# Kernel optimization log

Hardware: AMD Instinct MI355X
Metric: run time of the kernel (lower is better)

## Reference

```python
import jax, jax.numpy as jnp
import numpy as np

B, T, H, I, O = 256, 8192, 16, 1, 1


def setup_inputs() -> dict:
    key = jax.random.key(0)
    ks = jax.random.split(key, 8)
    s = 1.0 / np.sqrt(H)  # PyTorch default init scale
    x = jax.random.normal(ks[0], (B, T, I), dtype=jnp.float32)
    h0 = jax.random.normal(ks[1], (1, B, H), dtype=jnp.float32)
    W_ih = jax.random.uniform(ks[2], (H, I), jnp.float32, -s, s)
    W_hh = jax.random.uniform(ks[3], (H, H), jnp.float32, -s, s)
    b_ih = jax.random.uniform(ks[4], (H,), jnp.float32, -s, s)
    b_hh = jax.random.uniform(ks[5], (H,), jnp.float32, -s, s)
    W_out = jax.random.uniform(ks[6], (O, H), jnp.float32, -s, s)
    b_out = jax.random.uniform(ks[7], (O,), jnp.float32, -s, s)
    return {"x": x, "h0": h0, "W_ih": W_ih, "W_hh": W_hh,
            "b_ih": b_ih, "b_hh": b_hh, "W_out": W_out, "b_out": b_out}


def reference(x, h0, W_ih, W_hh, b_ih, b_hh, W_out, b_out):
    # Precompute input projection for all timesteps: [T, B, H]
    xp = jnp.einsum('bti,hi->tbh', x, W_ih) + b_ih + b_hh

    def step(h, xt):
        h_new = jnp.tanh(xt + h @ W_hh.T)  # [B, H]
        return h_new, h_new

    hT, outs = jax.lax.scan(step, h0[0], xp)  # hT: [B,H], outs: [T,B,H]
    out_flat = outs.transpose(1, 0, 2).reshape(-1, H)  # [B*T, H]
    out = (out_flat @ W_out.T + b_out)[None]  # [1, B*T, O]
    return out, hT[None]  # hidden: [1, B, H]
```

## Files before the change

### kernel.cpp

```cpp
#include <hip/hip_runtime.h>

#define ROTI(v, CTRL) __builtin_amdgcn_update_dpp(0, (v), (CTRL), 0xF, 0xF, true)
#define ROTF(x, CTRL) __int_as_float(__builtin_amdgcn_update_dpp(0, __float_as_int(x), (CTRL), 0xF, 0xF, true))

constexpr int T_LEN = 8192;
constexpr int BATCH = 256;
constexpr int HID   = 16;

#define MATVEC(a0_, a1_, a2_, a3_, p_, h_)                                              \
  asm("s_nop 1\n\t"                                                                     \
      "v_fmac_f32 %[a0], %[h], %[w0]\n\t"                                               \
      "v_mul_f32_dpp %[a1], %[h], %[w4] row_ror:4 row_mask:0xf bank_mask:0xf\n\t"       \
      "v_mul_f32_dpp %[a2], %[h], %[w8] row_ror:8 row_mask:0xf bank_mask:0xf\n\t"       \
      "v_mul_f32_dpp %[a3], %[h], %[w12] row_ror:12 row_mask:0xf bank_mask:0xf\n\t"     \
      "v_add_f32_dpp %[p], %[p], %[p] row_ror:8 row_mask:0xf bank_mask:0xf\n\t"         \
      "v_fmac_f32_dpp %[a0], %[h], %[w1] row_ror:1 row_mask:0xf bank_mask:0xf\n\t"      \
      "v_fmac_f32_dpp %[a1], %[h], %[w5] row_ror:5 row_mask:0xf bank_mask:0xf\n\t"      \
      "v_fmac_f32_dpp %[a2], %[h], %[w9] row_ror:9 row_mask:0xf bank_mask:0xf\n\t"      \
      "v_add_f32_dpp %[p], %[p], %[p] row_ror:4 row_mask:0xf bank_mask:0xf\n\t"         \
      "v_fmac_f32_dpp %[a3], %[h], %[w13] row_ror:13 row_mask:0xf bank_mask:0xf\n\t"    \
      "v_fmac_f32_dpp %[a0], %[h], %[w2] row_ror:2 row_mask:0xf bank_mask:0xf\n\t"      \
      "v_fmac_f32_dpp %[a1], %[h], %[w6] row_ror:6 row_mask:0xf bank_mask:0xf\n\t"      \
      "v_add_f32_dpp %[p], %[p], %[p] row_ror:2 row_mask:0xf bank_mask:0xf\n\t"         \
      "v_fmac_f32_dpp %[a2], %[h], %[w10] row_ror:10 row_mask:0xf bank_mask:0xf\n\t"    \
      "v_fmac_f32_dpp %[a3], %[h], %[w14] row_ror:14 row_mask:0xf bank_mask:0xf\n\t"    \
      "v_fmac_f32_dpp %[a0], %[h], %[w3] row_ror:3 row_mask:0xf bank_mask:0xf\n\t"      \
      "v_add_f32_dpp %[p], %[p], %[p] row_ror:1 row_mask:0xf bank_mask:0xf\n\t"         \
      "v_fmac_f32_dpp %[a1], %[h], %[w7] row_ror:7 row_mask:0xf bank_mask:0xf\n\t"      \
      "v_fmac_f32_dpp %[a2], %[h], %[w11] row_ror:11 row_mask:0xf bank_mask:0xf\n\t"    \
      "v_fmac_f32_dpp %[a3], %[h], %[w15] row_ror:15 row_mask:0xf bank_mask:0xf\n\t"    \
      : [a0]"+v"(a0_), [a1]"=&v"(a1_), [a2]"=&v"(a2_), [a3]"=&v"(a3_), [p]"+v"(p_)     \
      : [h]"v"(h_),                                                                     \
        [w0]"v"(wr[0]),  [w1]"v"(wr[1]),  [w2]"v"(wr[2]),  [w3]"v"(wr[3]),              \
        [w4]"v"(wr[4]),  [w5]"v"(wr[5]),  [w6]"v"(wr[6]),  [w7]"v"(wr[7]),              \
        [w8]"v"(wr[8]),  [w9]"v"(wr[9]),  [w10]"v"(wr[10]), [w11]"v"(wr[11]),           \
        [w12]"v"(wr[12]), [w13]"v"(wr[13]), [w14]"v"(wr[14]), [w15]"v"(wr[15]))

#define STEP(XV, LSEL) do {                                                             \
    float a0 = fmaf((XV), wih, bias), a1, a2, a3;                                       \
    MATVEC(a0, a1, a2, a3, p, h);                                                       \
    float o = p + bo;                                                                   \
    osel = (j == (LSEL)) ? o : osel;                                                    \
    float s = (a0 + a1) + (a2 + a3);                                                    \
    float e = __expf(s + s);                                                            \
    h = fmaf(-2.0f, __builtin_amdgcn_rcpf(e + 1.0f), 1.0f);                             \
    p = h * wout;                                                                       \
} while (0)

__global__ void __launch_bounds__(64, 1)
rnn_fused(const float* __restrict__ x,
          const float* __restrict__ h0,
          const float* __restrict__ Wih,
          const float* __restrict__ Whh,
          const float* __restrict__ bih,
          const float* __restrict__ bhh,
          const float* __restrict__ Wout,
          const float* __restrict__ boutp,
          float* __restrict__ out)
{
    const int lane = (int)threadIdx.x;
    const int j    = lane & 15;
    const int b    = (int)blockIdx.x * 4 + (lane >> 4);

    const int pr  = ROTI(j, 0x121);
    const int dir = (__builtin_amdgcn_readfirstlane(pr) == 1) ? 1 : -1;

    float wr[16];
#pragma unroll
    for (int r = 0; r < 16; ++r)
        wr[r] = Whh[j * HID + ((j + dir * r) & 15)];

    const float wih  = Wih[j];
    const float bias = bih[j] + bhh[j];
    const float wout = Wout[j];
    const float bo   = boutp[0];

    float h = h0[b * HID + j];
    float p = h * wout;
    float osel = 0.0f;

    const float* xb = x   + (size_t)b * T_LEN;
    float*       ob = out + (size_t)b * T_LEN;

    const float4* xv4 = (const float4*)xb;
    float4 c0 = xv4[0], c1 = xv4[1], c2 = xv4[2], c3 = xv4[3];

    for (int t = 0; t < T_LEN; t += 16) {
        const float4* nx = (const float4*)(xb + ((t + 16) & (T_LEN - 1)));
        float4 n0 = nx[0], n1 = nx[1], n2 = nx[2], n3 = nx[3];

        STEP(c0.x, 15);
        if (t > 0)
            ob[t - 16 + j] = osel;
        STEP(c0.y, 0);
        STEP(c0.z, 1);
        STEP(c0.w, 2);
        STEP(c1.x, 3);
        STEP(c1.y, 4);
        STEP(c1.z, 5);
        STEP(c1.w, 6);
        STEP(c2.x, 7);
        STEP(c2.y, 8);
        STEP(c2.z, 9);
        STEP(c2.w, 10);
        STEP(c3.x, 11);
        STEP(c3.y, 12);
        STEP(c3.z, 13);
        STEP(c3.w, 14);

        c0 = n0; c1 = n1; c2 = n2; c3 = n3;
    }

    p += ROTF(p, 0x128);
    p += ROTF(p, 0x124);
    p += ROTF(p, 0x122);
    p += ROTF(p, 0x121);
    float o_last = p + bo;
    osel = (j == 15) ? o_last : osel;
    ob[T_LEN - 16 + j] = osel;

    out[(size_t)BATCH * T_LEN + (size_t)b * HID + j] = h;
}

extern "C" void kernel_launch(void* const* d_in, const int* in_sizes, int n_in,
                              void* d_out, int out_size, void* d_ws, size_t ws_size,
                              hipStream_t stream)
{
    const float* x    = (const float*)d_in[0];
    const float* h0   = (const float*)d_in[1];
    const float* Wih  = (const float*)d_in[2];
    const float* Whh  = (const float*)d_in[3];
    const float* bih  = (const float*)d_in[4];
    const float* bhh  = (const float*)d_in[5];
    const float* Wout = (const float*)d_in[6];
    const float* bout = (const float*)d_in[7];
    float* out = (float*)d_out;

    rnn_fused<<<dim3(BATCH / 4), dim3(64), 0, stream>>>(
        x, h0, Wih, Whh, bih, bhh, Wout, bout, out);
}
```

Before: 599.0 us.

## Interleave four batch groups per wavefront to hide recurrence latency

Each 64-lane wavefront now processes four independent groups of four batch rows, interleaving their matvec/tanh chains within every timestep, and the grid is reduced accordingly. Input prefetch uses ping-pong register buffers and tanh uses exp2 with a prescaled argument. The goal is to fill the DPP/transcendental latency bubbles of a single serial recurrence with independent work, at the cost of using far fewer CUs and more registers per wave.

```diff
diff --git a/kernel.cpp b/kernel.cpp
--- a/kernel.cpp
+++ b/kernel.cpp
@@ -6,6 +6,7 @@
 constexpr int T_LEN = 8192;
 constexpr int BATCH = 256;
 constexpr int HID   = 16;
+constexpr int G     = 4;
 
 #define MATVEC(a0_, a1_, a2_, a3_, p_, h_)                                              \
   asm("s_nop 1\n\t"                                                                     \
@@ -36,17 +37,6 @@
         [w8]"v"(wr[8]),  [w9]"v"(wr[9]),  [w10]"v"(wr[10]), [w11]"v"(wr[11]),           \
         [w12]"v"(wr[12]), [w13]"v"(wr[13]), [w14]"v"(wr[14]), [w15]"v"(wr[15]))
 
-#define STEP(XV, LSEL) do {                                                             \
-    float a0 = fmaf((XV), wih, bias), a1, a2, a3;                                       \
-    MATVEC(a0, a1, a2, a3, p, h);                                                       \
-    float o = p + bo;                                                                   \
-    osel = (j == (LSEL)) ? o : osel;                                                    \
-    float s = (a0 + a1) + (a2 + a3);                                                    \
-    float e = __expf(s + s);                                                            \
-    h = fmaf(-2.0f, __builtin_amdgcn_rcpf(e + 1.0f), 1.0f);                             \
-    p = h * wout;                                                                       \
-} while (0)
-
 __global__ void __launch_bounds__(64, 1)
 rnn_fused(const float* __restrict__ x,
           const float* __restrict__ h0,
@@ -60,7 +50,7 @@
 {
     const int lane = (int)threadIdx.x;
     const int j    = lane & 15;
-    const int b    = (int)blockIdx.x * 4 + (lane >> 4);
+    const int g    = lane >> 4;
 
     const int pr  = ROTI(j, 0x121);
     const int dir = (__builtin_amdgcn_readfirstlane(pr) == 1) ? 1 : -1;
@@ -75,51 +65,84 @@
     const float wout = Wout[j];
     const float bo   = boutp[0];
 
-    float h = h0[b * HID + j];
-    float p = h * wout;
-    float osel = 0.0f;
-
-    const float* xb = x   + (size_t)b * T_LEN;
-    float*       ob = out + (size_t)b * T_LEN;
-
-    const float4* xv4 = (const float4*)xb;
-    float4 c0 = xv4[0], c1 = xv4[1], c2 = xv4[2], c3 = xv4[3];
-
-    for (int t = 0; t < T_LEN; t += 16) {
-        const float4* nx = (const float4*)(xb + ((t + 16) & (T_LEN - 1)));
-        float4 n0 = nx[0], n1 = nx[1], n2 = nx[2], n3 = nx[3];
-
-        STEP(c0.x, 15);
-        if (t > 0)
-            ob[t - 16 + j] = osel;
-        STEP(c0.y, 0);
-        STEP(c0.z, 1);
-        STEP(c0.w, 2);
-        STEP(c1.x, 3);
-        STEP(c1.y, 4);
-        STEP(c1.z, 5);
-        STEP(c1.w, 6);
-        STEP(c2.x, 7);
-        STEP(c2.y, 8);
-        STEP(c2.z, 9);
-        STEP(c2.w, 10);
-        STEP(c3.x, 11);
-        STEP(c3.y, 12);
-        STEP(c3.z, 13);
-        STEP(c3.w, 14);
-
-        c0 = n0; c1 = n1; c2 = n2; c3 = n3;
+    int    b[G];
+    float  h[G], p[G], osel[G];
+    const float* xb[G];
+    float*       ob[G];
+#pragma unroll
+    for (int s = 0; s < G; ++s) {
+        b[s]    = (int)blockIdx.x * 16 + s * 4 + g;
+        h[s]    = h0[b[s] * HID + j];
+        p[s]    = h[s] * wout;
+        osel[s] = 0.0f;
+        xb[s]   = x   + (size_t)b[s] * T_LEN;
+        ob[s]   = out + (size_t)b[s] * T_LEN;
     }
 
-    p += ROTF(p, 0x128);
-    p += ROTF(p, 0x124);
-    p += ROTF(p, 0x122);
-    p += ROTF(p, 0x121);
-    float o_last = p + bo;
-    osel = (j == 15) ? o_last : osel;
-    ob[T_LEN - 16 + j] = osel;
+    float bufA[G][16], bufB[G][16];
+#pragma unroll
+    for (int s = 0; s < G; ++s)
+#pragma unroll
+        for (int q = 0; q < 4; ++q) {
+            float4 v = *(const float4*)(xb[s] + 4 * q);
+            bufA[s][4*q+0] = v.x; bufA[s][4*q+1] = v.y;
+            bufA[s][4*q+2] = v.z; bufA[s][4*q+3] = v.w;
+        }
 
-    out[(size_t)BATCH * T_LEN + (size_t)b * HID + j] = h;
+    auto body = [&](int t, float (&cur)[G][16], float (&nxt)[G][16]) {
+        const int tn = (t + 16) & (T_LEN - 1);
+#pragma unroll
+        for (int s = 0; s < G; ++s)
+#pragma unroll
+            for (int q = 0; q < 4; ++q) {
+                float4 v = *(const float4*)(xb[s] + tn + 4 * q);
+                nxt[s][4*q+0] = v.x; nxt[s][4*q+1] = v.y;
+                nxt[s][4*q+2] = v.z; nxt[s][4*q+3] = v.w;
+            }
+
+#pragma unroll
+        for (int pos = 0; pos < 16; ++pos) {
+            const int LSEL = (pos + 15) & 15;
+            float a0[G], a1[G], a2[G], a3[G];
+#pragma unroll
+            for (int s = 0; s < G; ++s) {
+                a0[s] = fmaf(cur[s][pos], wih, bias);
+                MATVEC(a0[s], a1[s], a2[s], a3[s], p[s], h[s]);
+            }
+#pragma unroll
+            for (int s = 0; s < G; ++s) {
+                float o = p[s] + bo;
+                osel[s] = (j == LSEL) ? o : osel[s];
+                float sum = (a0[s] + a1[s]) + (a2[s] + a3[s]);
+                float e   = __builtin_amdgcn_exp2f(sum * 2.8853900817779268f);
+                h[s] = fmaf(-2.0f, __builtin_amdgcn_rcpf(e + 1.0f), 1.0f);
+                p[s] = h[s] * wout;
+            }
+            if (pos == 0 && t > 0) {
+#pragma unroll
+                for (int s = 0; s < G; ++s)
+                    ob[s][t - 16 + j] = osel[s];
+            }
+        }
+    };
+
+    for (int t = 0; t < T_LEN; t += 32) {
+        body(t,      bufA, bufB);
+        body(t + 16, bufB, bufA);
+    }
+
+#pragma unroll
+    for (int s = 0; s < G; ++s) {
+        float q = p[s];
+        q += ROTF(q, 0x128);
+        q += ROTF(q, 0x124);
+        q += ROTF(q, 0x122);
+        q += ROTF(q, 0x121);
+        float o_last = q + bo;
+        osel[s] = (j == 15) ? o_last : osel[s];
+        ob[s][T_LEN - 16 + j] = osel[s];
+        out[(size_t)BATCH * T_LEN + (size_t)b[s] * HID + j] = h[s];
+    }
 }
 
 extern "C" void kernel_launch(void* const* d_in, const int* in_sizes, int n_in,
@@ -136,6 +159,6 @@
     const float* bout = (const float*)d_in[7];
     float* out = (float*)d_out;
 
-    rnn_fused<<<dim3(BATCH / 4), dim3(64), 0, stream>>>(
+    rnn_fused<<<dim3(BATCH / 16), dim3(64), 0, stream>>>(
         x, h0, Wih, Whh, bih, bhh, Wout, bout, out);
 }
```

Result: slower. 2.140 ms (+257.2%).

## Interleave two independent batch chains per wavefront to hide recurrence latency

Applied to the files above, without the earlier changes.

Each wavefront now carries two independent recurrent chains (batches b and b+4) and interleaves their matvec, tanh and output steps, so one chain's dependent DPP and transcendental latency can overlap with the other's work. The grid is halved to 32 blocks, so fewer CUs are in use but each has more instruction-level parallelism. The time loop is unrolled by 32 with double-buffered input prefetch, and exp is computed directly with exp2 using a prescaled constant. The risk is that with only one wave per CU, the halved parallelism makes the serial chain per wave twice as long if the interleaving does not hide enough latency.

```diff
diff --git a/kernel.cpp b/kernel.cpp
--- a/kernel.cpp
+++ b/kernel.cpp
@@ -31,25 +31,53 @@
       "v_fmac_f32_dpp %[a3], %[h], %[w15] row_ror:15 row_mask:0xf bank_mask:0xf\n\t"    \
       : [a0]"+v"(a0_), [a1]"=&v"(a1_), [a2]"=&v"(a2_), [a3]"=&v"(a3_), [p]"+v"(p_)     \
       : [h]"v"(h_),                                                                     \
-        [w0]"v"(wr[0]),  [w1]"v"(wr[1]),  [w2]"v"(wr[2]),  [w3]"v"(wr[3]),              \
-        [w4]"v"(wr[4]),  [w5]"v"(wr[5]),  [w6]"v"(wr[6]),  [w7]"v"(wr[7]),              \
-        [w8]"v"(wr[8]),  [w9]"v"(wr[9]),  [w10]"v"(wr[10]), [w11]"v"(wr[11]),           \
-        [w12]"v"(wr[12]), [w13]"v"(wr[13]), [w14]"v"(wr[14]), [w15]"v"(wr[15]))
+        [w0]"v"(wr0),  [w1]"v"(wr1),  [w2]"v"(wr2),  [w3]"v"(wr3),                      \
+        [w4]"v"(wr4),  [w5]"v"(wr5),  [w6]"v"(wr6),  [w7]"v"(wr7),                      \
+        [w8]"v"(wr8),  [w9]"v"(wr9),  [w10]"v"(wr10), [w11]"v"(wr11),                   \
+        [w12]"v"(wr12), [w13]"v"(wr13), [w14]"v"(wr14), [w15]"v"(wr15))
 
-#define STEP(XV, LSEL) do {                                                             \
-    float a0 = fmaf((XV), wih, bias), a1, a2, a3;                                       \
-    MATVEC(a0, a1, a2, a3, p, h);                                                       \
-    float o = p + bo;                                                                   \
-    osel = (j == (LSEL)) ? o : osel;                                                    \
-    float s = (a0 + a1) + (a2 + a3);                                                    \
-    float e = __expf(s + s);                                                            \
-    h = fmaf(-2.0f, __builtin_amdgcn_rcpf(e + 1.0f), 1.0f);                             \
-    p = h * wout;                                                                       \
+#define STEP2(XV0, XV1, LSEL) do {                                                      \
+    float a00 = fmaf((XV0), wih, bias), a10, a20, a30;                                  \
+    float a01 = fmaf((XV1), wih, bias), a11, a21, a31;                                  \
+    MATVEC(a00, a10, a20, a30, p0, hh0);                                                \
+    MATVEC(a01, a11, a21, a31, p1, hh1);                                                \
+    float o0 = p0 + bo;                                                                 \
+    float o1 = p1 + bo;                                                                 \
+    osel0 = (j == (LSEL)) ? o0 : osel0;                                                 \
+    osel1 = (j == (LSEL)) ? o1 : osel1;                                                 \
+    float s0 = (a00 + a10) + (a20 + a30);                                               \
+    float s1 = (a01 + a11) + (a21 + a31);                                               \
+    float e0 = __builtin_amdgcn_exp2f(s0 * 2.8853900817779268f);                        \
+    float e1 = __builtin_amdgcn_exp2f(s1 * 2.8853900817779268f);                        \
+    hh0 = fmaf(-2.0f, __builtin_amdgcn_rcpf(e0 + 1.0f), 1.0f);                          \
+    hh1 = fmaf(-2.0f, __builtin_amdgcn_rcpf(e1 + 1.0f), 1.0f);                          \
+    p0 = hh0 * wout;                                                                    \
+    p1 = hh1 * wout;                                                                    \
+} while (0)
+
+#define BLOCK16(tb, Q0, Q1, Q2, Q3, R0, R1, R2, R3) do {                                \
+    STEP2(Q0.x, R0.x, 15);                                                              \
+    if ((tb) > 0) { ob0[(tb) - 16 + j] = osel0; ob1[(tb) - 16 + j] = osel1; }           \
+    STEP2(Q0.y, R0.y, 0);                                                               \
+    STEP2(Q0.z, R0.z, 1);                                                               \
+    STEP2(Q0.w, R0.w, 2);                                                               \
+    STEP2(Q1.x, R1.x, 3);                                                               \
+    STEP2(Q1.y, R1.y, 4);                                                               \
+    STEP2(Q1.z, R1.z, 5);                                                               \
+    STEP2(Q1.w, R1.w, 6);                                                               \
+    STEP2(Q2.x, R2.x, 7);                                                               \
+    STEP2(Q2.y, R2.y, 8);                                                               \
+    STEP2(Q2.z, R2.z, 9);                                                               \
+    STEP2(Q2.w, R2.w, 10);                                                              \
+    STEP2(Q3.x, R3.x, 11);                                                              \
+    STEP2(Q3.y, R3.y, 12);                                                              \
+    STEP2(Q3.z, R3.z, 13);                                                              \
+    STEP2(Q3.w, R3.w, 14);                                                              \
 } while (0)
 
 __global__ void __launch_bounds__(64, 1)
 rnn_fused(const float* __restrict__ x,
-          const float* __restrict__ h0,
+          const float* __restrict__ hinit,
           const float* __restrict__ Wih,
           const float* __restrict__ Whh,
           const float* __restrict__ bih,
@@ -60,66 +88,92 @@
 {
     const int lane = (int)threadIdx.x;
     const int j    = lane & 15;
-    const int b    = (int)blockIdx.x * 4 + (lane >> 4);
+    const int g    = lane >> 4;
 
     const int pr  = ROTI(j, 0x121);
     const int dir = (__builtin_amdgcn_readfirstlane(pr) == 1) ? 1 : -1;
 
-    float wr[16];
-#pragma unroll
-    for (int r = 0; r < 16; ++r)
-        wr[r] = Whh[j * HID + ((j + dir * r) & 15)];
+    float wr0  = Whh[j * HID + ((j + dir * 0)  & 15)];
+    float wr1  = Whh[j * HID + ((j + dir * 1)  & 15)];
+    float wr2  = Whh[j * HID + ((j + dir * 2)  & 15)];
+    float wr3  = Whh[j * HID + ((j + dir * 3)  & 15)];
+    float wr4  = Whh[j * HID + ((j + dir * 4)  & 15)];
+    float wr5  = Whh[j * HID + ((j + dir * 5)  & 15)];
+    float wr6  = Whh[j * HID + ((j + dir * 6)  & 15)];
+    float wr7  = Whh[j * HID + ((j + dir * 7)  & 15)];
+    float wr8  = Whh[j * HID + ((j + dir * 8)  & 15)];
+    float wr9  = Whh[j * HID + ((j + dir * 9)  & 15)];
+    float wr10 = Whh[j * HID + ((j + dir * 10) & 15)];
+    float wr11 = Whh[j * HID + ((j + dir * 11) & 15)];
+    float wr12 = Whh[j * HID + ((j + dir * 12) & 15)];
+    float wr13 = Whh[j * HID + ((j + dir * 13) & 15)];
+    float wr14 = Whh[j * HID + ((j + dir * 14) & 15)];
+    float wr15 = Whh[j * HID + ((j + dir * 15) & 15)];
 
     const float wih  = Wih[j];
     const float bias = bih[j] + bhh[j];
     const float wout = Wout[j];
     const float bo   = boutp[0];
 
-    float h = h0[b * HID + j];
-    float p = h * wout;
-    float osel = 0.0f;
+    const int b0 = (int)blockIdx.x * 8 + g;
+    const int b1 = b0 + 4;
 
-    const float* xb = x   + (size_t)b * T_LEN;
-    float*       ob = out + (size_t)b * T_LEN;
+    float hh0 = hinit[b0 * HID + j];
+    float hh1 = hinit[b1 * HID + j];
+    float p0 = hh0 * wout;
+    float p1 = hh1 * wout;
+    float osel0 = 0.0f, osel1 = 0.0f;
 
-    const float4* xv4 = (const float4*)xb;
-    float4 c0 = xv4[0], c1 = xv4[1], c2 = xv4[2], c3 = xv4[3];
+    const float* xb0 = x   + (size_t)b0 * T_LEN;
+    const float* xb1 = x   + (size_t)b1 * T_LEN;
+    float*       ob0 = out + (size_t)b0 * T_LEN;
+    float*       ob1 = out + (size_t)b1 * T_LEN;
 
-    for (int t = 0; t < T_LEN; t += 16) {
-        const float4* nx = (const float4*)(xb + ((t + 16) & (T_LEN - 1)));
-        float4 n0 = nx[0], n1 = nx[1], n2 = nx[2], n3 = nx[3];
+    float4 A0 = ((const float4*)xb0)[0], A1 = ((const float4*)xb0)[1],
+           A2 = ((const float4*)xb0)[2], A3 = ((const float4*)xb0)[3];
+    float4 C0 = ((const float4*)xb1)[0], C1 = ((const float4*)xb1)[1],
+           C2 = ((const float4*)xb1)[2], C3 = ((const float4*)xb1)[3];
+    float4 B0, B1, B2, B3, D0, D1, D2, D3;
 
-        STEP(c0.x, 15);
-        if (t > 0)
-            ob[t - 16 + j] = osel;
-        STEP(c0.y, 0);
-        STEP(c0.z, 1);
-        STEP(c0.w, 2);
-        STEP(c1.x, 3);
-        STEP(c1.y, 4);
-        STEP(c1.z, 5);
-        STEP(c1.w, 6);
-        STEP(c2.x, 7);
-        STEP(c2.y, 8);
-        STEP(c2.z, 9);
-        STEP(c2.w, 10);
-        STEP(c3.x, 11);
-        STEP(c3.y, 12);
-        STEP(c3.z, 13);
-        STEP(c3.w, 14);
+    for (int t = 0; t < T_LEN; t += 32) {
+        {
+            const float* q0 = xb0 + t + 16;
+            const float* q1 = xb1 + t + 16;
+            B0 = ((const float4*)q0)[0]; B1 = ((const float4*)q0)[1];
+            B2 = ((const float4*)q0)[2]; B3 = ((const float4*)q0)[3];
+            D0 = ((const float4*)q1)[0]; D1 = ((const float4*)q1)[1];
+            D2 = ((const float4*)q1)[2]; D3 = ((const float4*)q1)[3];
+        }
+        BLOCK16(t, A0, A1, A2, A3, C0, C1, C2, C3);
 
-        c0 = n0; c1 = n1; c2 = n2; c3 = n3;
+        {
+            const int tn = (t + 32) & (T_LEN - 1);
+            const float* q0 = xb0 + tn;
+            const float* q1 = xb1 + tn;
+            A0 = ((const float4*)q0)[0]; A1 = ((const float4*)q0)[1];
+            A2 = ((const float4*)q0)[2]; A3 = ((const float4*)q0)[3];
+            C0 = ((const float4*)q1)[0]; C1 = ((const float4*)q1)[1];
+            C2 = ((const float4*)q1)[2]; C3 = ((const float4*)q1)[3];
+        }
+        BLOCK16(t + 16, B0, B1, B2, B3, D0, D1, D2, D3);
     }
 
-    p += ROTF(p, 0x128);
-    p += ROTF(p, 0x124);
-    p += ROTF(p, 0x122);
-    p += ROTF(p, 0x121);
-    float o_last = p + bo;
-    osel = (j == 15) ? o_last : osel;
-    ob[T_LEN - 16 + j] = osel;
-
-    out[(size_t)BATCH * T_LEN + (size_t)b * HID + j] = h;
+    {
+        float q = p0;
+        q += ROTF(q, 0x128); q += ROTF(q, 0x124);
+        q += ROTF(q, 0x122); q += ROTF(q, 0x121);
+        osel0 = (j == 15) ? (q + bo) : osel0;
+        ob0[T_LEN - 16 + j] = osel0;
+        out[(size_t)BATCH * T_LEN + (size_t)b0 * HID + j] = hh0;
+    }
+    {
+        float q = p1;
+        q += ROTF(q, 0x128); q += ROTF(q, 0x124);
+        q += ROTF(q, 0x122); q += ROTF(q, 0x121);
+        osel1 = (j == 15) ? (q + bo) : osel1;
+        ob1[T_LEN - 16 + j] = osel1;
+        out[(size_t)BATCH * T_LEN + (size_t)b1 * HID + j] = hh1;
+    }
 }
 
 extern "C" void kernel_launch(void* const* d_in, const int* in_sizes, int n_in,
@@ -136,6 +190,6 @@
     const float* bout = (const float*)d_in[7];
     float* out = (float*)d_out;
 
-    rnn_fused<<<dim3(BATCH / 4), dim3(64), 0, stream>>>(
+    rnn_fused<<<dim3(BATCH / 8), dim3(64), 0, stream>>>(
         x, h0, Wih, Whh, bih, bhh, Wout, bout, out);
 }
```

New measurement: 1.093 ms. 1.82x slower.

## Offload output projection to a consumer wavefront via an LDS ring buffer

Applied to the files above, without the earlier changes.

Splits each block into a producer wavefront that runs the recurrence and a consumer wavefront that computes the output projection. Hidden states pass between them through a shared-memory ring buffer with spin-wait counters. This takes the per-step DPP reduction and output select off the serial critical path. It also folds the 2*log2(e) factor into the weights so tanh can use exp2 directly. The cost is LDS stores on every step, spin-wait synchronisation, and a second wavefront competing for issue slots.

```diff
diff --git a/kernel.cpp b/kernel.cpp
--- a/kernel.cpp
+++ b/kernel.cpp
@@ -1,55 +1,58 @@
 #include <hip/hip_runtime.h>
 
 #define ROTI(v, CTRL) __builtin_amdgcn_update_dpp(0, (v), (CTRL), 0xF, 0xF, true)
-#define ROTF(x, CTRL) __int_as_float(__builtin_amdgcn_update_dpp(0, __float_as_int(x), (CTRL), 0xF, 0xF, true))
 
-constexpr int T_LEN = 8192;
-constexpr int BATCH = 256;
-constexpr int HID   = 16;
+constexpr int T_LEN  = 8192;
+constexpr int BATCH  = 256;
+constexpr int HID    = 16;
+constexpr int RING   = 128;
+constexpr int SLOT_W = 68;
+constexpr int CHUNK  = 32;
 
-#define MATVEC(a0_, a1_, a2_, a3_, p_, h_)                                              \
+#define MATVEC(a0_, a1_, a2_, a3_, h_)                                                  \
   asm("s_nop 1\n\t"                                                                     \
       "v_fmac_f32 %[a0], %[h], %[w0]\n\t"                                               \
       "v_mul_f32_dpp %[a1], %[h], %[w4] row_ror:4 row_mask:0xf bank_mask:0xf\n\t"       \
       "v_mul_f32_dpp %[a2], %[h], %[w8] row_ror:8 row_mask:0xf bank_mask:0xf\n\t"       \
       "v_mul_f32_dpp %[a3], %[h], %[w12] row_ror:12 row_mask:0xf bank_mask:0xf\n\t"     \
-      "v_add_f32_dpp %[p], %[p], %[p] row_ror:8 row_mask:0xf bank_mask:0xf\n\t"         \
       "v_fmac_f32_dpp %[a0], %[h], %[w1] row_ror:1 row_mask:0xf bank_mask:0xf\n\t"      \
       "v_fmac_f32_dpp %[a1], %[h], %[w5] row_ror:5 row_mask:0xf bank_mask:0xf\n\t"      \
       "v_fmac_f32_dpp %[a2], %[h], %[w9] row_ror:9 row_mask:0xf bank_mask:0xf\n\t"      \
-      "v_add_f32_dpp %[p], %[p], %[p] row_ror:4 row_mask:0xf bank_mask:0xf\n\t"         \
       "v_fmac_f32_dpp %[a3], %[h], %[w13] row_ror:13 row_mask:0xf bank_mask:0xf\n\t"    \
       "v_fmac_f32_dpp %[a0], %[h], %[w2] row_ror:2 row_mask:0xf bank_mask:0xf\n\t"      \
       "v_fmac_f32_dpp %[a1], %[h], %[w6] row_ror:6 row_mask:0xf bank_mask:0xf\n\t"      \
-      "v_add_f32_dpp %[p], %[p], %[p] row_ror:2 row_mask:0xf bank_mask:0xf\n\t"         \
       "v_fmac_f32_dpp %[a2], %[h], %[w10] row_ror:10 row_mask:0xf bank_mask:0xf\n\t"    \
       "v_fmac_f32_dpp %[a3], %[h], %[w14] row_ror:14 row_mask:0xf bank_mask:0xf\n\t"    \
       "v_fmac_f32_dpp %[a0], %[h], %[w3] row_ror:3 row_mask:0xf bank_mask:0xf\n\t"      \
-      "v_add_f32_dpp %[p], %[p], %[p] row_ror:1 row_mask:0xf bank_mask:0xf\n\t"         \
       "v_fmac_f32_dpp %[a1], %[h], %[w7] row_ror:7 row_mask:0xf bank_mask:0xf\n\t"      \
       "v_fmac_f32_dpp %[a2], %[h], %[w11] row_ror:11 row_mask:0xf bank_mask:0xf\n\t"    \
       "v_fmac_f32_dpp %[a3], %[h], %[w15] row_ror:15 row_mask:0xf bank_mask:0xf\n\t"    \
-      : [a0]"+v"(a0_), [a1]"=&v"(a1_), [a2]"=&v"(a2_), [a3]"=&v"(a3_), [p]"+v"(p_)     \
+      : [a0]"+v"(a0_), [a1]"=&v"(a1_), [a2]"=&v"(a2_), [a3]"=&v"(a3_)                  \
       : [h]"v"(h_),                                                                     \
-        [w0]"v"(wr[0]),  [w1]"v"(wr[1]),  [w2]"v"(wr[2]),  [w3]"v"(wr[3]),              \
-        [w4]"v"(wr[4]),  [w5]"v"(wr[5]),  [w6]"v"(wr[6]),  [w7]"v"(wr[7]),              \
-        [w8]"v"(wr[8]),  [w9]"v"(wr[9]),  [w10]"v"(wr[10]), [w11]"v"(wr[11]),           \
-        [w12]"v"(wr[12]), [w13]"v"(wr[13]), [w14]"v"(wr[14]), [w15]"v"(wr[15]))
+        [w0]"v"(wr0),  [w1]"v"(wr1),  [w2]"v"(wr2),  [w3]"v"(wr3),                      \
+        [w4]"v"(wr4),  [w5]"v"(wr5),  [w6]"v"(wr6),  [w7]"v"(wr7),                      \
+        [w8]"v"(wr8),  [w9]"v"(wr9),  [w10]"v"(wr10), [w11]"v"(wr11),                   \
+        [w12]"v"(wr12), [w13]"v"(wr13), [w14]"v"(wr14), [w15]"v"(wr15))
 
-#define STEP(XV, LSEL) do {                                                             \
-    float a0 = fmaf((XV), wih, bias), a1, a2, a3;                                       \
-    MATVEC(a0, a1, a2, a3, p, h);                                                       \
-    float o = p + bo;                                                                   \
-    osel = (j == (LSEL)) ? o : osel;                                                    \
+#define STEP(XV) do {                                                                   \
+    float a0 = fmaf((XV), wihK, biasK), a1, a2, a3;                                     \
+    MATVEC(a0, a1, a2, a3, h);                                                          \
     float s = (a0 + a1) + (a2 + a3);                                                    \
-    float e = __expf(s + s);                                                            \
+    float e = __builtin_amdgcn_exp2f(s);                                                \
     h = fmaf(-2.0f, __builtin_amdgcn_rcpf(e + 1.0f), 1.0f);                             \
-    p = h * wout;                                                                       \
+    *rp = h; rp += SLOT_W;                                                              \
 } while (0)
 
-__global__ void __launch_bounds__(64, 1)
+#define BLOCK16(C0, C1, C2, C3) do {                                                    \
+    STEP(C0.x); STEP(C0.y); STEP(C0.z); STEP(C0.w);                                     \
+    STEP(C1.x); STEP(C1.y); STEP(C1.z); STEP(C1.w);                                     \
+    STEP(C2.x); STEP(C2.y); STEP(C2.z); STEP(C2.w);                                     \
+    STEP(C3.x); STEP(C3.y); STEP(C3.z); STEP(C3.w);                                     \
+} while (0)
+
+__global__ void __launch_bounds__(128, 1)
 rnn_fused(const float* __restrict__ x,
-          const float* __restrict__ h0,
+          const float* __restrict__ hinit,
           const float* __restrict__ Wih,
           const float* __restrict__ Whh,
           const float* __restrict__ bih,
@@ -58,68 +61,115 @@
           const float* __restrict__ boutp,
           float* __restrict__ out)
 {
-    const int lane = (int)threadIdx.x;
-    const int j    = lane & 15;
-    const int b    = (int)blockIdx.x * 4 + (lane >> 4);
+    __shared__ float ring[RING * SLOT_W];
+    __shared__ int   syncc[2];
+    volatile int* prodc = &syncc[0];
+    volatile int* consc = &syncc[1];
 
-    const int pr  = ROTI(j, 0x121);
-    const int dir = (__builtin_amdgcn_readfirstlane(pr) == 1) ? 1 : -1;
+    const int tid = (int)threadIdx.x;
+    if (tid == 0) { syncc[0] = 0; syncc[1] = 0; }
+    __syncthreads();
 
-    float wr[16];
-#pragma unroll
-    for (int r = 0; r < 16; ++r)
-        wr[r] = Whh[j * HID + ((j + dir * r) & 15)];
+    if (tid < 64) {
+        const int j = tid & 15;
+        const int g = tid >> 4;
+        const int b = (int)blockIdx.x * 4 + g;
 
-    const float wih  = Wih[j];
-    const float bias = bih[j] + bhh[j];
-    const float wout = Wout[j];
-    const float bo   = boutp[0];
+        const int pr  = ROTI(j, 0x121);
+        const int dir = (__builtin_amdgcn_readfirstlane(pr) == 1) ? 1 : -1;
 
-    float h = h0[b * HID + j];
-    float p = h * wout;
-    float osel = 0.0f;
+        const float K2 = 2.8853900817779268f;
+        float wr0  = K2 * Whh[j * HID + ((j + dir * 0)  & 15)];
+        float wr1  = K2 * Whh[j * HID + ((j + dir * 1)  & 15)];
+        float wr2  = K2 * Whh[j * HID + ((j + dir * 2)  & 15)];
+        float wr3  = K2 * Whh[j * HID + ((j + dir * 3)  & 15)];
+        float wr4  = K2 * Whh[j * HID + ((j + dir * 4)  & 15)];
+        float wr5  = K2 * Whh[j * HID + ((j + dir * 5)  & 15)];
+        float wr6  = K2 * Whh[j * HID + ((j + dir * 6)  & 15)];
+        float wr7  = K2 * Whh[j * HID + ((j + dir * 7)  & 15)];
+        float wr8  = K2 * Whh[j * HID + ((j + dir * 8)  & 15)];
+        float wr9  = K2 * Whh[j * HID + ((j + dir * 9)  & 15)];
+        float wr10 = K2 * Whh[j * HID + ((j + dir * 10) & 15)];
+        float wr11 = K2 * Whh[j * HID + ((j + dir * 11) & 15)];
+        float wr12 = K2 * Whh[j * HID + ((j + dir * 12) & 15)];
+        float wr13 = K2 * Whh[j * HID + ((j + dir * 13) & 15)];
+        float wr14 = K2 * Whh[j * HID + ((j + dir * 14) & 15)];
+        float wr15 = K2 * Whh[j * HID + ((j + dir * 15) & 15)];
 
-    const float* xb = x   + (size_t)b * T_LEN;
-    float*       ob = out + (size_t)b * T_LEN;
+        const float wihK  = K2 * Wih[j];
+        const float biasK = K2 * (bih[j] + bhh[j]);
 
-    const float4* xv4 = (const float4*)xb;
-    float4 c0 = xv4[0], c1 = xv4[1], c2 = xv4[2], c3 = xv4[3];
+        float h = hinit[b * HID + j];
+        const float* xb = x + (size_t)b * T_LEN;
 
-    for (int t = 0; t < T_LEN; t += 16) {
-        const float4* nx = (const float4*)(xb + ((t + 16) & (T_LEN - 1)));
-        float4 n0 = nx[0], n1 = nx[1], n2 = nx[2], n3 = nx[3];
+        float4 c0 = ((const float4*)xb)[0], c1 = ((const float4*)xb)[1],
+               c2 = ((const float4*)xb)[2], c3 = ((const float4*)xb)[3];
 
-        STEP(c0.x, 15);
-        if (t > 0)
-            ob[t - 16 + j] = osel;
-        STEP(c0.y, 0);
-        STEP(c0.z, 1);
-        STEP(c0.w, 2);
-        STEP(c1.x, 3);
-        STEP(c1.y, 4);
-        STEP(c1.z, 5);
-        STEP(c1.w, 6);
-        STEP(c2.x, 7);
-        STEP(c2.y, 8);
-        STEP(c2.z, 9);
-        STEP(c2.w, 10);
-        STEP(c3.x, 11);
-        STEP(c3.y, 12);
-        STEP(c3.z, 13);
-        STEP(c3.w, 14);
+        for (int t0 = 0; t0 < T_LEN; t0 += 16) {
+            if ((t0 & (CHUNK - 1)) == 0) {
+                const int need = t0 + CHUNK - RING;
+                if (need > 0) {
+                    while (*consc < need) { }
+                    __asm__ volatile("" ::: "memory");
+                }
+            }
+            const int tn = (t0 + 16) & (T_LEN - 1);
+            const float* q = xb + tn;
+            float4 n0 = ((const float4*)q)[0], n1 = ((const float4*)q)[1],
+                   n2 = ((const float4*)q)[2], n3 = ((const float4*)q)[3];
 
-        c0 = n0; c1 = n1; c2 = n2; c3 = n3;
+            float* rp = &ring[(t0 & (RING - 1)) * SLOT_W + g * 17 + j];
+            BLOCK16(c0, c1, c2, c3);
+            c0 = n0; c1 = n1; c2 = n2; c3 = n3;
+
+            if (((t0 + 16) & (CHUNK - 1)) == 0) {
+                __asm__ volatile("s_waitcnt lgkmcnt(0)" ::: "memory");
+                *prodc = t0 + 16;
+            }
+        }
+
+        out[(size_t)BATCH * T_LEN + (size_t)b * HID + j] = h;
+    } else {
+        const int lane = tid - 64;
+        const int tt   = lane & 15;
+        const int bs   = lane >> 4;
+        const int bg   = (int)blockIdx.x * 4 + bs;
+
+        const float w0  = Wout[0],  w1  = Wout[1],  w2  = Wout[2],  w3  = Wout[3];
+        const float w4  = Wout[4],  w5  = Wout[5],  w6  = Wout[6],  w7  = Wout[7];
+        const float w8  = Wout[8],  w9  = Wout[9],  w10 = Wout[10], w11 = Wout[11];
+        const float w12 = Wout[12], w13 = Wout[13], w14 = Wout[14], w15 = Wout[15];
+        const float bo  = boutp[0];
+
+        float* ob = out + (size_t)bg * T_LEN;
+
+        for (int t0 = 0; t0 < T_LEN; t0 += 16) {
+            while (*prodc < t0 + 16) { }
+            __asm__ volatile("" ::: "memory");
+
+            const float* hr = &ring[((t0 + tt) & (RING - 1)) * SLOT_W + bs * 17];
+            float o = bo;
+            o = fmaf(hr[0],  w0,  o);
+            o = fmaf(hr[1],  w1,  o);
+            o = fmaf(hr[2],  w2,  o);
+            o = fmaf(hr[3],  w3,  o);
+            o = fmaf(hr[4],  w4,  o);
+            o = fmaf(hr[5],  w5,  o);
+            o = fmaf(hr[6],  w6,  o);
+            o = fmaf(hr[7],  w7,  o);
+            o = fmaf(hr[8],  w8,  o);
+            o = fmaf(hr[9],  w9,  o);
+            o = fmaf(hr[10], w10, o);
+            o = fmaf(hr[11], w11, o);
+            o = fmaf(hr[12], w12, o);
+            o = fmaf(hr[13], w13, o);
+            o = fmaf(hr[14], w14, o);
+            o = fmaf(hr[15], w15, o);
+            ob[t0 + tt] = o;
+
+            *consc = t0 + 16;
+        }
     }
-
-    p += ROTF(p, 0x128);
-    p += ROTF(p, 0x124);
-    p += ROTF(p, 0x122);
-    p += ROTF(p, 0x121);
-    float o_last = p + bo;
-    osel = (j == 15) ? o_last : osel;
-    ob[T_LEN - 16 + j] = osel;
-
-    out[(size_t)BATCH * T_LEN + (size_t)b * HID + j] = h;
 }
 
 extern "C" void kernel_launch(void* const* d_in, const int* in_sizes, int n_in,
@@ -136,6 +186,6 @@
     const float* bout = (const float*)d_in[7];
     float* out = (float*)d_out;
 
-    rnn_fused<<<dim3(BATCH / 4), dim3(64), 0, stream>>>(
+    rnn_fused<<<dim3(BATCH / 4), dim3(128), 0, stream>>>(
         x, h0, Wih, Whh, bih, bhh, Wout, bout, out);
 }
```

After: 541.7 us. -9.6%, faster.
